# Optimization experiments

Hardware: AMD Instinct MI355X
Metric: run time of the kernel (lower is better)

Reference implementation:

```python
import jax, jax.numpy as jnp
import numpy as np

B, T, D, E, P = 4, 2048, 1024, 8, 1024

def setup_inputs() -> dict:
    key = jax.random.key(0)
    k1, k2, k3 = jax.random.split(key, 3)
    x = jax.random.normal(k1, (B, T, D), dtype=jnp.float32)
    gate_w = jax.random.normal(k2, (D, E), dtype=jnp.float32) * (1.0 / np.sqrt(D))
    gate_b = jnp.zeros((E,), dtype=jnp.float32)
    expert_w = jax.random.normal(k3, (E, D, P), dtype=jnp.float32) * (1.0 / np.sqrt(D))
    expert_b = jnp.zeros((E, P), dtype=jnp.float32)
    return {"x": x, "gate_w": gate_w, "gate_b": gate_b,
            "expert_w": expert_w, "expert_b": expert_b}

def reference(x, gate_w, gate_b, expert_w, expert_b):
    # gating: Dense(E) with softmax -> [B, T, E]
    gate = jax.nn.softmax(jnp.einsum('btd,de->bte', x, gate_w) + gate_b, axis=-1)
    # all experts as one batched GEMM: [B, T, E, P]
    expert_out = jnp.einsum('btd,edp->btep', x, expert_w) + expert_b
    # gate-weighted sum over experts -> [B, T, P]
    out = jnp.einsum('bte,btep->btp', gate, expert_out)
    return out
```

## Files before the change

### kernel.cpp

```cpp
#include <hip/hip_runtime.h>
#include <hip/hip_bf16.h>
#include <math.h>

#define M_TOT 8192
#define D_DIM 1024
#define E_NUM 8
#define P_DIM 1024
#define K_TOT (E_NUM * D_DIM)

typedef __attribute__((ext_vector_type(8))) short short8;
typedef __attribute__((ext_vector_type(4))) float f32x4;
typedef __attribute__((ext_vector_type(8))) unsigned short u16x8;

static __device__ __forceinline__ unsigned short f2bf(float f) {
  unsigned u = __builtin_bit_cast(unsigned, f);
  unsigned r = (u + 0x7fffu + ((u >> 16) & 1u)) >> 16;
  return (unsigned short)r;
}

__global__ __launch_bounds__(256) void gate_kernel(const float* __restrict__ x,
                                                   const float* __restrict__ gw,
                                                   const float* __restrict__ gb,
                                                   float* __restrict__ gate) {
  const int row  = blockIdx.x * 4 + (threadIdx.x >> 6);
  const int lane = threadIdx.x & 63;
  const float* xr = x + (size_t)row * D_DIM;
  float acc[E_NUM];
#pragma unroll
  for (int e = 0; e < E_NUM; ++e) acc[e] = 0.f;
#pragma unroll
  for (int it = 0; it < 16; ++it) {
    const int d = it * 64 + lane;
    const float xv = xr[d];
    const float4* g4 = reinterpret_cast<const float4*>(gw + (size_t)d * E_NUM);
    float4 a = g4[0], b = g4[1];
    acc[0] += xv * a.x; acc[1] += xv * a.y; acc[2] += xv * a.z; acc[3] += xv * a.w;
    acc[4] += xv * b.x; acc[5] += xv * b.y; acc[6] += xv * b.z; acc[7] += xv * b.w;
  }
#pragma unroll
  for (int off = 32; off >= 1; off >>= 1) {
#pragma unroll
    for (int e = 0; e < E_NUM; ++e) acc[e] += __shfl_xor(acc[e], off, 64);
  }
  if (lane == 0) {
    float v[E_NUM], mx = -1e30f;
#pragma unroll
    for (int e = 0; e < E_NUM; ++e) { v[e] = acc[e] + gb[e]; mx = fmaxf(mx, v[e]); }
    float s = 0.f;
#pragma unroll
    for (int e = 0; e < E_NUM; ++e) { v[e] = expf(v[e] - mx); s += v[e]; }
    const float inv = 1.f / s;
#pragma unroll
    for (int e = 0; e < E_NUM; ++e) gate[(size_t)row * E_NUM + e] = v[e] * inv;
  }
}

__global__ __launch_bounds__(256) void wtrans2_kernel(const float* __restrict__ w,
                                                      unsigned short* __restrict__ wt) {
  __shared__ float tile[64][65];
  const int e  = blockIdx.z;
  const int p0 = blockIdx.y * 64;
  const int d0 = blockIdx.x * 64;
  const int tx = threadIdx.x & 63;
  const int ty = threadIdx.x >> 6;
  const float* src = w + ((size_t)e * D_DIM + d0) * P_DIM + p0;
#pragma unroll
  for (int i = 0; i < 16; ++i) {
    const int dr = i * 4 + ty;
    tile[dr][tx] = src[(size_t)dr * P_DIM + tx];
  }
  __syncthreads();
#pragma unroll
  for (int i = 0; i < 16; ++i) {
    const int pr = i * 4 + ty;
    const int c = tx ^ ((pr & 7) << 3);
    wt[(size_t)(p0 + pr) * K_TOT + e * D_DIM + d0 + c] = f2bf(tile[tx][pr]);
  }
}

__global__ __launch_bounds__(256) void aprep_kernel(const float* __restrict__ x,
                                                    const float* __restrict__ gate,
                                                    unsigned short* __restrict__ ap) {
  const int tid = threadIdx.x;
  const int m   = blockIdx.x * 2 + (tid >> 7);
  const int jd  = tid & 127;
  const float4* xp = reinterpret_cast<const float4*>(x + (size_t)m * D_DIM + jd * 8);
  const float4 p = xp[0], q = xp[1];
  unsigned short* row = ap + (size_t)m * K_TOT;
  const int cbase = (jd >> 3) * 8 + ((jd & 7) ^ (m & 7));
#pragma unroll
  for (int e = 0; e < E_NUM; ++e) {
    const float gs = gate[(size_t)m * E_NUM + e];
    u16x8 v;
    v[0] = f2bf(p.x * gs); v[1] = f2bf(p.y * gs);
    v[2] = f2bf(p.z * gs); v[3] = f2bf(p.w * gs);
    v[4] = f2bf(q.x * gs); v[5] = f2bf(q.y * gs);
    v[6] = f2bf(q.z * gs); v[7] = f2bf(q.w * gs);
    *reinterpret_cast<u16x8*>(&row[(size_t)(e * 128 + cbase) * 8]) = v;
  }
}

__global__ __launch_bounds__(256, 4) void gemm_sk3_kernel(
    const unsigned short* __restrict__ ap,
    const unsigned short* __restrict__ wt,
    const float* __restrict__ gate,
    const float* __restrict__ eb,
    float* __restrict__ out) {
  __shared__ unsigned short lA[128 * 64];
  __shared__ unsigned short lB[128 * 64];
  __shared__ float lG[128 * 8];

  const int tid  = threadIdx.x;
  const int lane = tid & 63;
  const int wid  = tid >> 6;
  const int wr   = wid >> 1, wc = wid & 1;

  const int bid = blockIdx.x;
  const int xcd = bid & 7, idx = bid >> 3;
  const int kh  = idx & 1;
  const int nt  = (idx >> 1) & 7;
  const int mt  = xcd * 8 + (idx >> 4);
  const int m0  = mt * 128, n0 = nt * 128;

  reinterpret_cast<float4*>(lG)[tid] =
      reinterpret_cast<const float4*>(gate + (size_t)m0 * E_NUM)[tid];

  f32x4 acc[4][4];
#pragma unroll
  for (int i = 0; i < 4; ++i)
#pragma unroll
    for (int j = 0; j < 4; ++j)
#pragma unroll
      for (int k = 0; k < 4; ++k) acc[i][j][k] = 0.f;

  const int r0 = tid >> 3;
  const int c8 = tid & 7;
  const unsigned short* pA = ap + (size_t)(m0 + r0) * K_TOT + (size_t)kh * 4096 + c8 * 8;
  const unsigned short* pB = wt + (size_t)(n0 + r0) * K_TOT + (size_t)kh * 4096 + c8 * 8;

  for (int kt = 0; kt < 64; ++kt) {
    __syncthreads();
#pragma unroll
    for (int i = 0; i < 4; ++i) {
      __builtin_amdgcn_global_load_lds(
          (const __attribute__((address_space(1))) void*)(pA + (size_t)i * 32 * K_TOT),
          (__attribute__((address_space(3))) void*)&lA[(tid + i * 256) * 8], 16, 0, 0);
    }
#pragma unroll
    for (int i = 0; i < 4; ++i) {
      __builtin_amdgcn_global_load_lds(
          (const __attribute__((address_space(1))) void*)(pB + (size_t)i * 32 * K_TOT),
          (__attribute__((address_space(3))) void*)&lB[(tid + i * 256) * 8], 16, 0, 0);
    }
    __syncthreads();
#pragma unroll
    for (int kk = 0; kk < 2; ++kk) {
      const int e0 = kk * 32 + (lane >> 4) * 8;
      short8 a[4], b[4];
#pragma unroll
      for (int m = 0; m < 4; ++m) {
        const int r = wr * 64 + m * 16 + (lane & 15);
        a[m] = *reinterpret_cast<const short8*>(&lA[r * 64 + (e0 ^ ((r & 7) << 3))]);
      }
#pragma unroll
      for (int n = 0; n < 4; ++n) {
        const int r = wc * 64 + n * 16 + (lane & 15);
        b[n] = *reinterpret_cast<const short8*>(&lB[r * 64 + (e0 ^ ((r & 7) << 3))]);
      }
#pragma unroll
      for (int m = 0; m < 4; ++m)
#pragma unroll
        for (int n = 0; n < 4; ++n)
          acc[m][n] = __builtin_amdgcn_mfma_f32_16x16x32_bf16(a[m], b[n], acc[m][n], 0, 0, 0);
    }
    pA += 64;
    pB += 64;
  }

#pragma unroll
  for (int n = 0; n < 4; ++n) {
    const int cl = wc * 64 + n * 16 + (lane & 15);
    float lb[E_NUM];
    if (kh == 0) {
#pragma unroll
      for (int e = 0; e < E_NUM; ++e) lb[e] = eb[(size_t)e * P_DIM + n0 + cl];
    }
#pragma unroll
    for (int m = 0; m < 4; ++m) {
#pragma unroll
      for (int reg = 0; reg < 4; ++reg) {
        const int r = wr * 64 + m * 16 + (lane >> 4) * 4 + reg;
        float v = acc[m][n][reg];
        if (kh == 0) {
          float bsum = 0.f;
#pragma unroll
          for (int e = 0; e < E_NUM; ++e) bsum += lG[r * 8 + e] * lb[e];
          v += bsum;
        }
        atomicAdd(&out[(size_t)(m0 + r) * P_DIM + n0 + cl], v);
      }
    }
  }
}


__global__ __launch_bounds__(256) void wtrans_kernel(const float* __restrict__ w,
                                                     unsigned short* __restrict__ wt) {
  __shared__ float tile[64][65];
  const int e  = blockIdx.z;
  const int p0 = blockIdx.y * 64;
  const int d0 = blockIdx.x * 64;
  const int tx = threadIdx.x & 63;
  const int ty = threadIdx.x >> 6;
  const float* src = w + ((size_t)e * D_DIM + d0) * P_DIM + p0;
#pragma unroll
  for (int i = 0; i < 16; ++i) {
    const int dr = i * 4 + ty;
    tile[dr][tx] = src[(size_t)dr * P_DIM + tx];
  }
  __syncthreads();
  unsigned short* dst = wt + ((size_t)e * P_DIM + p0) * D_DIM + d0;
#pragma unroll
  for (int i = 0; i < 16; ++i) {
    const int pr = i * 4 + ty;
    const int cc = tx ^ ((pr & 7) << 3);
    dst[(size_t)pr * D_DIM + cc] = f2bf(tile[tx][pr]);
  }
}

__global__ __launch_bounds__(256, 2) void moe_gemm_kernel(
    const float* __restrict__ x,
    const unsigned short* __restrict__ wt,
    const float* __restrict__ gate,
    const float* __restrict__ eb,
    float* __restrict__ out) {
  __shared__ unsigned short lA[128 * 64];
  __shared__ unsigned short lB[128 * 64];
  __shared__ float lG[128 * 8];
  __shared__ float lBias[E_NUM * 128];

  const int tid  = threadIdx.x;
  const int lane = tid & 63;
  const int wid  = tid >> 6;
  const int wr   = wid >> 1, wc = wid & 1;
  const int m0   = blockIdx.x * 128;
  const int n0   = blockIdx.y * 128;

  reinterpret_cast<float4*>(lG)[tid] =
      reinterpret_cast<const float4*>(gate + (size_t)m0 * E_NUM)[tid];
  {
    const int e = tid >> 5, cc = (tid & 31) * 4;
    *reinterpret_cast<float4*>(&lBias[e * 128 + cc]) =
        *reinterpret_cast<const float4*>(&eb[(size_t)e * P_DIM + n0 + cc]);
  }
  __syncthreads();

  const int rA   = tid >> 1;
  const int colA = (tid & 1) * 32;
  const float* xrow = x + (size_t)(m0 + rA) * D_DIM + colA;

  f32x4 acc[4][4];
#pragma unroll
  for (int i = 0; i < 4; ++i)
#pragma unroll
    for (int jj = 0; jj < 4; ++jj)
#pragma unroll
      for (int k = 0; k < 4; ++k) acc[i][jj][k] = 0.f;

  for (int e = 0; e < E_NUM; ++e) {
    const float gs = lG[rA * 8 + e];
    const unsigned short* wte = wt + ((size_t)e * P_DIM + n0) * D_DIM;
    for (int kt = 0; kt < 16; ++kt) {
      __syncthreads();
      const float4* apv = reinterpret_cast<const float4*>(xrow + kt * 64);
#pragma unroll
      for (int jj = 0; jj < 4; ++jj) {
        float4 p = apv[2 * jj], q = apv[2 * jj + 1];
        u16x8 v;
        v[0] = f2bf(p.x * gs); v[1] = f2bf(p.y * gs);
        v[2] = f2bf(p.z * gs); v[3] = f2bf(p.w * gs);
        v[4] = f2bf(q.x * gs); v[5] = f2bf(q.y * gs);
        v[6] = f2bf(q.z * gs); v[7] = f2bf(q.w * gs);
        const int idx = rA * 64 + ((colA + jj * 8) ^ ((rA & 7) << 3));
        *reinterpret_cast<u16x8*>(&lA[idx]) = v;
      }
#pragma unroll
      for (int i = 0; i < 4; ++i) {
        const int u  = tid + i * 256;
        const int rr = u >> 3;
        const int cc = u & 7;
        const unsigned short* src = wte + (size_t)rr * D_DIM + kt * 64 + cc * 8;
        __builtin_amdgcn_global_load_lds(
            (const __attribute__((address_space(1))) void*)src,
            (__attribute__((address_space(3))) void*)&lB[u * 8], 16, 0, 0);
      }
      __syncthreads();
#pragma unroll
      for (int kk = 0; kk < 2; ++kk) {
        const int e0 = kk * 32 + (lane >> 4) * 8;
        short8 a[4], b[4];
#pragma unroll
        for (int m = 0; m < 4; ++m) {
          const int r = wr * 64 + m * 16 + (lane & 15);
          a[m] = *reinterpret_cast<const short8*>(&lA[r * 64 + (e0 ^ ((r & 7) << 3))]);
        }
#pragma unroll
        for (int n = 0; n < 4; ++n) {
          const int r = wc * 64 + n * 16 + (lane & 15);
          b[n] = *reinterpret_cast<const short8*>(&lB[r * 64 + (e0 ^ ((r & 7) << 3))]);
        }
#pragma unroll
        for (int m = 0; m < 4; ++m)
#pragma unroll
          for (int n = 0; n < 4; ++n)
            acc[m][n] = __builtin_amdgcn_mfma_f32_16x16x32_bf16(a[m], b[n], acc[m][n], 0, 0, 0);
      }
    }
  }

#pragma unroll
  for (int m = 0; m < 4; ++m) {
#pragma unroll
    for (int n = 0; n < 4; ++n) {
      const int rbase = wr * 64 + m * 16 + ((lane >> 4) * 4);
      const int cl    = wc * 64 + n * 16 + (lane & 15);
#pragma unroll
      for (int reg = 0; reg < 4; ++reg) {
        const int r = rbase + reg;
        float bsum = 0.f;
#pragma unroll
        for (int e = 0; e < E_NUM; ++e) bsum += lG[r * 8 + e] * lBias[e * 128 + cl];
        out[(size_t)(m0 + r) * P_DIM + n0 + cl] = acc[m][n][reg] + bsum;
      }
    }
  }
}


extern "C" void kernel_launch(void* const* d_in, const int* in_sizes, int n_in,
                              void* d_out, int out_size, void* d_ws, size_t ws_size,
                              hipStream_t stream) {
  const float* x  = (const float*)d_in[0];
  const float* gw = (const float*)d_in[1];
  const float* gb = (const float*)d_in[2];
  const float* ew = (const float*)d_in[3];
  const float* eb = (const float*)d_in[4];
  float* out = (float*)d_out;

  char* ws = (char*)d_ws;
  float* gate        = (float*)ws;
  unsigned short* wt = (unsigned short*)(ws + 262144);

  const size_t need_big = 262144ull + 16777216ull + 134217728ull;

  gate_kernel<<<M_TOT / 4, 256, 0, stream>>>(x, gw, gb, gate);

  if (ws_size >= need_big) {
    unsigned short* apb = (unsigned short*)(ws + 262144 + 16777216);
    hipMemsetAsync(d_out, 0, (size_t)out_size * sizeof(float), stream);
    wtrans2_kernel<<<dim3(D_DIM / 64, P_DIM / 64, E_NUM), 256, 0, stream>>>(ew, wt);
    aprep_kernel<<<M_TOT / 2, 256, 0, stream>>>(x, gate, apb);
    gemm_sk3_kernel<<<1024, 256, 0, stream>>>(apb, wt, gate, eb, out);
  } else {
    wtrans_kernel<<<dim3(D_DIM / 64, P_DIM / 64, E_NUM), 256, 0, stream>>>(ew, wt);
    moe_gemm_kernel<<<dim3(M_TOT / 128, P_DIM / 128), 256, 0, stream>>>(x, wt, gate, eb, out);
  }
}
```

Measured before the change: 206.3 us.

## Apply gate scaling in GEMM accumulators instead of materializing gated activations

Replaces the per-expert gated activation buffer with a single bf16 copy of x and folds the gate weights into the GEMM by rescaling accumulators with consecutive gate ratios between experts, then multiplying by the last gate at the end. This removes writing and reading a large expanded A matrix, leaving the GEMM reading a far smaller buffer. The block-to-tile mapping is also changed. Dividing by small gate values risks precision loss or overflow in the ratio rescaling.

```diff
diff --git a/kernel.cpp b/kernel.cpp
--- a/kernel.cpp
+++ b/kernel.cpp
@@ -78,30 +78,22 @@
   }
 }
 
-__global__ __launch_bounds__(256) void aprep_kernel(const float* __restrict__ x,
-                                                    const float* __restrict__ gate,
-                                                    unsigned short* __restrict__ ap) {
+__global__ __launch_bounds__(256) void xb_kernel(const float* __restrict__ x,
+                                                 unsigned short* __restrict__ xb) {
   const int tid = threadIdx.x;
   const int m   = blockIdx.x * 2 + (tid >> 7);
   const int jd  = tid & 127;
   const float4* xp = reinterpret_cast<const float4*>(x + (size_t)m * D_DIM + jd * 8);
   const float4 p = xp[0], q = xp[1];
-  unsigned short* row = ap + (size_t)m * K_TOT;
   const int cbase = (jd >> 3) * 8 + ((jd & 7) ^ (m & 7));
-#pragma unroll
-  for (int e = 0; e < E_NUM; ++e) {
-    const float gs = gate[(size_t)m * E_NUM + e];
-    u16x8 v;
-    v[0] = f2bf(p.x * gs); v[1] = f2bf(p.y * gs);
-    v[2] = f2bf(p.z * gs); v[3] = f2bf(p.w * gs);
-    v[4] = f2bf(q.x * gs); v[5] = f2bf(q.y * gs);
-    v[6] = f2bf(q.z * gs); v[7] = f2bf(q.w * gs);
-    *reinterpret_cast<u16x8*>(&row[(size_t)(e * 128 + cbase) * 8]) = v;
-  }
-}
-
-__global__ __launch_bounds__(256, 4) void gemm_sk3_kernel(
-    const unsigned short* __restrict__ ap,
+  u16x8 v;
+  v[0] = f2bf(p.x); v[1] = f2bf(p.y); v[2] = f2bf(p.z); v[3] = f2bf(p.w);
+  v[4] = f2bf(q.x); v[5] = f2bf(q.y); v[6] = f2bf(q.z); v[7] = f2bf(q.w);
+  *reinterpret_cast<u16x8*>(&xb[(size_t)m * D_DIM + cbase * 8]) = v;
+}
+
+__global__ __launch_bounds__(256, 4) void gemm_ex_kernel(
+    const unsigned short* __restrict__ xb,
     const unsigned short* __restrict__ wt,
     const float* __restrict__ gate,
     const float* __restrict__ eb,
@@ -116,10 +108,10 @@
   const int wr   = wid >> 1, wc = wid & 1;
 
   const int bid = blockIdx.x;
-  const int xcd = bid & 7, idx = bid >> 3;
+  const int nt  = bid & 7;
+  const int idx = bid >> 3;
   const int kh  = idx & 1;
-  const int nt  = (idx >> 1) & 7;
-  const int mt  = xcd * 8 + (idx >> 4);
+  const int mt  = idx >> 1;
   const int m0  = mt * 128, n0 = nt * 128;
 
   reinterpret_cast<float4*>(lG)[tid] =
@@ -135,46 +127,60 @@
 
   const int r0 = tid >> 3;
   const int c8 = tid & 7;
-  const unsigned short* pA = ap + (size_t)(m0 + r0) * K_TOT + (size_t)kh * 4096 + c8 * 8;
-  const unsigned short* pB = wt + (size_t)(n0 + r0) * K_TOT + (size_t)kh * 4096 + c8 * 8;
-
-  for (int kt = 0; kt < 64; ++kt) {
-    __syncthreads();
-#pragma unroll
-    for (int i = 0; i < 4; ++i) {
-      __builtin_amdgcn_global_load_lds(
-          (const __attribute__((address_space(1))) void*)(pA + (size_t)i * 32 * K_TOT),
-          (__attribute__((address_space(3))) void*)&lA[(tid + i * 256) * 8], 16, 0, 0);
-    }
-#pragma unroll
-    for (int i = 0; i < 4; ++i) {
-      __builtin_amdgcn_global_load_lds(
-          (const __attribute__((address_space(1))) void*)(pB + (size_t)i * 32 * K_TOT),
-          (__attribute__((address_space(3))) void*)&lB[(tid + i * 256) * 8], 16, 0, 0);
-    }
-    __syncthreads();
-#pragma unroll
-    for (int kk = 0; kk < 2; ++kk) {
-      const int e0 = kk * 32 + (lane >> 4) * 8;
-      short8 a[4], b[4];
+  const unsigned short* pAb = xb + (size_t)(m0 + r0) * D_DIM + c8 * 8;
+  const unsigned short* pBb = wt + (size_t)(n0 + r0) * K_TOT + c8 * 8;
+
+  for (int e = 0; e < 4; ++e) {
+    const int eg = kh * 4 + e;
+    if (e > 0) {
 #pragma unroll
       for (int m = 0; m < 4; ++m) {
-        const int r = wr * 64 + m * 16 + (lane & 15);
-        a[m] = *reinterpret_cast<const short8*>(&lA[r * 64 + (e0 ^ ((r & 7) << 3))]);
-      }
-#pragma unroll
-      for (int n = 0; n < 4; ++n) {
-        const int r = wc * 64 + n * 16 + (lane & 15);
-        b[n] = *reinterpret_cast<const short8*>(&lB[r * 64 + (e0 ^ ((r & 7) << 3))]);
-      }
-#pragma unroll
-      for (int m = 0; m < 4; ++m)
-#pragma unroll
-        for (int n = 0; n < 4; ++n)
-          acc[m][n] = __builtin_amdgcn_mfma_f32_16x16x32_bf16(a[m], b[n], acc[m][n], 0, 0, 0);
-    }
-    pA += 64;
-    pB += 64;
+#pragma unroll
+        for (int reg = 0; reg < 4; ++reg) {
+          const int r = wr * 64 + m * 16 + (lane >> 4) * 4 + reg;
+          const float ratio = lG[r * 8 + (eg - 1)] / lG[r * 8 + eg];
+#pragma unroll
+          for (int n = 0; n < 4; ++n) acc[m][n][reg] *= ratio;
+        }
+      }
+    }
+    const unsigned short* pB = pBb + (size_t)eg * D_DIM;
+    for (int kt = 0; kt < 16; ++kt) {
+      __syncthreads();
+#pragma unroll
+      for (int i = 0; i < 4; ++i) {
+        __builtin_amdgcn_global_load_lds(
+            (const __attribute__((address_space(1))) void*)(pAb + (size_t)i * 32 * D_DIM + kt * 64),
+            (__attribute__((address_space(3))) void*)&lA[(tid + i * 256) * 8], 16, 0, 0);
+      }
+#pragma unroll
+      for (int i = 0; i < 4; ++i) {
+        __builtin_amdgcn_global_load_lds(
+            (const __attribute__((address_space(1))) void*)(pB + (size_t)i * 32 * K_TOT + kt * 64),
+            (__attribute__((address_space(3))) void*)&lB[(tid + i * 256) * 8], 16, 0, 0);
+      }
+      __syncthreads();
+#pragma unroll
+      for (int kk = 0; kk < 2; ++kk) {
+        const int e0 = kk * 32 + (lane >> 4) * 8;
+        short8 a[4], b[4];
+#pragma unroll
+        for (int m = 0; m < 4; ++m) {
+          const int r = wr * 64 + m * 16 + (lane & 15);
+          a[m] = *reinterpret_cast<const short8*>(&lA[r * 64 + (e0 ^ ((r & 7) << 3))]);
+        }
+#pragma unroll
+        for (int n = 0; n < 4; ++n) {
+          const int r = wc * 64 + n * 16 + (lane & 15);
+          b[n] = *reinterpret_cast<const short8*>(&lB[r * 64 + (e0 ^ ((r & 7) << 3))]);
+        }
+#pragma unroll
+        for (int m = 0; m < 4; ++m)
+#pragma unroll
+          for (int n = 0; n < 4; ++n)
+            acc[m][n] = __builtin_amdgcn_mfma_f32_16x16x32_bf16(a[m], b[n], acc[m][n], 0, 0, 0);
+      }
+    }
   }
 
 #pragma unroll
@@ -189,8 +195,9 @@
     for (int m = 0; m < 4; ++m) {
 #pragma unroll
       for (int reg = 0; reg < 4; ++reg) {
-        const int r = wr * 64 + m * 16 + (lane >> 4) * 4 + reg;
-        float v = acc[m][n][reg];
+        const int r  = wr * 64 + m * 16 + (lane >> 4) * 4 + reg;
+        const float gl = lG[r * 8 + kh * 4 + 3];
+        float v = acc[m][n][reg] * gl;
         if (kh == 0) {
           float bsum = 0.f;
 #pragma unroll
@@ -351,16 +358,16 @@
   float* gate        = (float*)ws;
   unsigned short* wt = (unsigned short*)(ws + 262144);
 
-  const size_t need_big = 262144ull + 16777216ull + 134217728ull;
+  const size_t need_new = 262144ull + 16777216ull + 16777216ull;
 
   gate_kernel<<<M_TOT / 4, 256, 0, stream>>>(x, gw, gb, gate);
 
-  if (ws_size >= need_big) {
-    unsigned short* apb = (unsigned short*)(ws + 262144 + 16777216);
+  if (ws_size >= need_new) {
+    unsigned short* xbb = (unsigned short*)(ws + 262144 + 16777216);
     hipMemsetAsync(d_out, 0, (size_t)out_size * sizeof(float), stream);
     wtrans2_kernel<<<dim3(D_DIM / 64, P_DIM / 64, E_NUM), 256, 0, stream>>>(ew, wt);
-    aprep_kernel<<<M_TOT / 2, 256, 0, stream>>>(x, gate, apb);
-    gemm_sk3_kernel<<<1024, 256, 0, stream>>>(apb, wt, gate, eb, out);
+    xb_kernel<<<M_TOT / 2, 256, 0, stream>>>(x, xbb);
+    gemm_ex_kernel<<<1024, 256, 0, stream>>>(xbb, wt, gate, eb, out);
   } else {
     wtrans_kernel<<<dim3(D_DIM / 64, P_DIM / 64, E_NUM), 256, 0, stream>>>(ew, wt);
     moe_gemm_kernel<<<dim3(M_TOT / 128, P_DIM / 128), 256, 0, stream>>>(x, wt, gate, eb, out);
```

New measurement: 190.1 us. -7.8%, faster.
